# Performance work log

Hardware: AMD Instinct MI355X
Metric: run time of the kernel (lower is better)

## Reference

```python
import jax, jax.numpy as jnp
import numpy as np

N = 100000
E = 1600000
IN_DIM = 64
HID = 64


def _glorot(key, shape):
    fan_in, fan_out = shape[0], shape[1]
    lim = np.sqrt(6.0 / (fan_in + fan_out))
    return jax.random.uniform(key, shape, jnp.float32, -lim, lim)


def setup_inputs() -> dict:
    key = jax.random.key(0)
    ks = jax.random.split(key, 14)
    x = jax.random.normal(ks[0], (N, IN_DIM), jnp.float32)
    edge_index = jax.random.randint(ks[1], (2, E), 0, N, jnp.int64)
    dims = [(IN_DIM, HID), (HID, HID), (HID, HID), (HID, 1)]
    inp = {"x": x, "edge_index": edge_index}
    for i, (di, do) in enumerate(dims, start=1):
        inp[f"Wself{i}"] = _glorot(ks[2 + 3 * (i - 1)], (di, do))
        inp[f"Wneigh{i}"] = _glorot(ks[3 + 3 * (i - 1)], (di, do))
        inp[f"b{i}"] = jnp.zeros((do,), jnp.float32)
    return inp


def _gn_block(h, src, dst, deg_inv, Wself, Wneigh, b, act):
    # gather -> scatter-add -> mean -> dense transform (GraphConv-style)
    msg = h[src]                                           # [E, d]
    agg = jax.ops.segment_sum(msg, dst, num_segments=N)    # [N, d]
    agg = agg * deg_inv                                    # mean aggregation
    out = h @ Wself + agg @ Wneigh + b
    return act(out)


def reference(x, edge_index, Wself1, Wneigh1, b1, Wself2, Wneigh2, b2,
              Wself3, Wneigh3, b3, Wself4, Wneigh4, b4):
    src, dst = edge_index[0], edge_index[1]
    deg = jax.ops.segment_sum(jnp.ones((E,), x.dtype), dst, num_segments=N)
    deg_inv = (1.0 / jnp.maximum(deg, 1.0))[:, None]       # [N, 1]
    relu = jax.nn.relu
    h = _gn_block(x, src, dst, deg_inv, Wself1, Wneigh1, b1, relu)
    h = _gn_block(h, src, dst, deg_inv, Wself2, Wneigh2, b2, relu)
    h = _gn_block(h, src, dst, deg_inv, Wself3, Wneigh3, b3, relu)
    h = _gn_block(h, src, dst, deg_inv, Wself4, Wneigh4, b4, lambda z: z)
    return jax.nn.sigmoid(h)                               # [N, 1]
```

## Files before the change

### kernel.cpp

```cpp
#include <hip/hip_runtime.h>
#include <hip/hip_bf16.h>
#include <math.h>


using bfrag = __attribute__((ext_vector_type(8))) short;
using ffrag = __attribute__((ext_vector_type(4))) float;

#define BKT_SHIFT 9
#define BKT_NODES (1 << BKT_SHIFT)

__device__ __forceinline__ int load_idx32(const int* __restrict__ ei32, int is64,
                                          long long pos) {
    return is64 ? ei32[2 * pos] : ei32[pos];
}

__device__ __forceinline__ unsigned short f2b_rne(float f) {
    union { float f; unsigned u; } c;
    c.f = f;
    unsigned r = c.u + 0x7FFFu + ((c.u >> 16) & 1u);
    return (unsigned short)(r >> 16);
}

__device__ __forceinline__ float b2f(unsigned short u) {
    union { unsigned u; float f; } c;
    c.u = ((unsigned)u) << 16;
    return c.f;
}

__global__ void bprep_init_kernel(
    const float* __restrict__ Ws1, const float* __restrict__ Wn1,
    const float* __restrict__ Ws2, const float* __restrict__ Wn2,
    const float* __restrict__ Ws3, const float* __restrict__ Wn3,
    unsigned short* __restrict__ bthi, unsigned short* __restrict__ btlo,
    const int* __restrict__ ei, int* __restrict__ bktc, int* __restrict__ flag) {
    if (blockIdx.x == 0) {
        bktc[threadIdx.x] = 0;
        if (threadIdx.x == 0) {
            int allz = 1;
            for (int i = 0; i < 32; ++i)
                if (ei[2 * i + 1] != 0) allz = 0;
            *flag = allz;
        }
    }
    int i = blockIdx.x * 256 + threadIdx.x;
    if (i >= 3 * 8192) return;
    int layer = i >> 13;
    int j = i & 8191;
    int n = j >> 7, k = j & 127;
    const float* Ws = layer == 0 ? Ws1 : (layer == 1 ? Ws2 : Ws3);
    const float* Wn = layer == 0 ? Wn1 : (layer == 1 ? Wn2 : Wn3);
    float v = (k < 64) ? Ws[k * 64 + n] : Wn[(k - 64) * 64 + n];
    unsigned short hi = f2b_rne(v);
    bthi[i] = hi;
    btlo[i] = f2b_rne(v - b2f(hi));
}

__global__ void split_x_kernel(const float4* __restrict__ in, ushort4* __restrict__ hi,
                               int n4) {
    int i = blockIdx.x * blockDim.x + threadIdx.x;
    if (i >= n4) return;
    float4 v = in[i];
    ushort4 h;
    h.x = f2b_rne(v.x); h.y = f2b_rne(v.y); h.z = f2b_rne(v.z); h.w = f2b_rne(v.w);
    hi[i] = h;
}

__global__ __launch_bounds__(256) void binA_kernel(
    const int* __restrict__ ei32, const int* __restrict__ flagp,
    int* __restrict__ bktCnt, unsigned* __restrict__ bins, int E, int nbkt,
    int cap, int chunksz) {
    __shared__ int cnt[256];
    __shared__ int base[256];
    int is64 = *flagp;
    int elo = blockIdx.x * chunksz;
    int ehi = min(E, elo + chunksz);
    if (elo >= E) return;
    for (int i = threadIdx.x; i < nbkt; i += 256) cnt[i] = 0;
    __syncthreads();
    for (int e = elo + (int)threadIdx.x; e < ehi; e += 256) {
        int dst = load_idx32(ei32, is64, (long long)E + e);
        atomicAdd(&cnt[dst >> BKT_SHIFT], 1);
    }
    __syncthreads();
    for (int i = threadIdx.x; i < nbkt; i += 256) {
        base[i] = atomicAdd(&bktCnt[i], cnt[i]);
        cnt[i] = 0;
    }
    __syncthreads();
    for (int e = elo + (int)threadIdx.x; e < ehi; e += 256) {
        int dst = load_idx32(ei32, is64, (long long)E + e);
        int src = load_idx32(ei32, is64, e);
        int b = dst >> BKT_SHIFT;
        int r = atomicAdd(&cnt[b], 1);
        bins[(size_t)b * cap + base[b] + r] =
            ((unsigned)(dst & (BKT_NODES - 1)) << 23) | (unsigned)src;
    }
}

__global__ __launch_bounds__(256) void bucketCSR_kernel(
    const int* __restrict__ bktCnt, const unsigned* __restrict__ bins,
    int* __restrict__ off, int* __restrict__ offe, int* __restrict__ col,
    float* __restrict__ dinv, int N, int cap) {
    __shared__ int deg[BKT_NODES];
    __shared__ int loc[BKT_NODES];
    __shared__ int ssum[256];
    int b = blockIdx.x;
    int lo = b << BKT_SHIFT;
    int n = min(BKT_NODES, N - lo);
    for (int i = threadIdx.x; i < BKT_NODES; i += 256) deg[i] = 0;
    __syncthreads();
    int cnt = bktCnt[b];
    const unsigned* bb = bins + (size_t)b * cap;
    for (int i = threadIdx.x; i < cnt; i += 256)
        atomicAdd(&deg[bb[i] >> 23], 1);
    __syncthreads();
    int t = threadIdx.x;
    int d0 = deg[2 * t], d1 = deg[2 * t + 1];
    int s = d0 + d1;
    ssum[t] = s;
    __syncthreads();
    for (int o = 1; o < 256; o <<= 1) {
        int v = (t >= o) ? ssum[t - o] : 0;
        __syncthreads();
        ssum[t] += v;
        __syncthreads();
    }
    int excl = ssum[t] - s;
    loc[2 * t] = excl;
    loc[2 * t + 1] = excl + d0;
    __syncthreads();
    int base = b * cap;
    for (int i = threadIdx.x; i < n; i += 256) {
        int d = deg[i];
        off[lo + i] = base + loc[i];
        offe[lo + i] = base + loc[i] + d;
        dinv[lo + i] = 1.0f / fmaxf((float)d, 1.0f);
    }
    __syncthreads();
    for (int i = threadIdx.x; i < cnt; i += 256) {
        unsigned p = bb[i];
        int pos = atomicAdd(&loc[p >> 23], 1);
        col[base + pos] = (int)(p & 0x7FFFFFu);
    }
}

__global__ __launch_bounds__(256) void gather64_b16_kernel(
    const unsigned short* __restrict__ hb, const int* __restrict__ off,
    const int* __restrict__ offe, const int* __restrict__ col,
    const float* __restrict__ dinv, unsigned short* __restrict__ ghi, int N) {
    int wave = threadIdx.x >> 6;
    int lane = threadIdx.x & 63;
    int g = lane >> 4;
    int t = lane & 15;
    int n = blockIdx.x * 4 + wave;
    if (n >= N) return;
    int e = off[n], end = offe[n];
    float4 a0 = make_float4(0.f, 0.f, 0.f, 0.f);
    float4 a1 = make_float4(0.f, 0.f, 0.f, 0.f);
    float4 a2 = make_float4(0.f, 0.f, 0.f, 0.f);
    float4 a3 = make_float4(0.f, 0.f, 0.f, 0.f);
    for (; e + 16 <= end; e += 16) {
        int s0 = col[e + g];
        int s1 = col[e + 4 + g];
        int s2 = col[e + 8 + g];
        int s3 = col[e + 12 + g];
        ushort4 u0 = *(const ushort4*)&hb[(size_t)s0 * 64 + t * 4];
        ushort4 u1 = *(const ushort4*)&hb[(size_t)s1 * 64 + t * 4];
        ushort4 u2 = *(const ushort4*)&hb[(size_t)s2 * 64 + t * 4];
        ushort4 u3 = *(const ushort4*)&hb[(size_t)s3 * 64 + t * 4];
        a0.x += b2f(u0.x); a0.y += b2f(u0.y); a0.z += b2f(u0.z); a0.w += b2f(u0.w);
        a1.x += b2f(u1.x); a1.y += b2f(u1.y); a1.z += b2f(u1.z); a1.w += b2f(u1.w);
        a2.x += b2f(u2.x); a2.y += b2f(u2.y); a2.z += b2f(u2.z); a2.w += b2f(u2.w);
        a3.x += b2f(u3.x); a3.y += b2f(u3.y); a3.z += b2f(u3.z); a3.w += b2f(u3.w);
    }
    for (; e + 8 <= end; e += 8) {
        int s0 = col[e + g];
        int s1 = col[e + 4 + g];
        ushort4 u0 = *(const ushort4*)&hb[(size_t)s0 * 64 + t * 4];
        ushort4 u1 = *(const ushort4*)&hb[(size_t)s1 * 64 + t * 4];
        a0.x += b2f(u0.x); a0.y += b2f(u0.y); a0.z += b2f(u0.z); a0.w += b2f(u0.w);
        a1.x += b2f(u1.x); a1.y += b2f(u1.y); a1.z += b2f(u1.z); a1.w += b2f(u1.w);
    }
    for (; e < end; e += 4) {
        if (e + g < end) {
            int s0 = col[e + g];
            ushort4 u0 = *(const ushort4*)&hb[(size_t)s0 * 64 + t * 4];
            a2.x += b2f(u0.x); a2.y += b2f(u0.y); a2.z += b2f(u0.z); a2.w += b2f(u0.w);
        }
    }
    float4 acc;
    acc.x = (a0.x + a1.x) + (a2.x + a3.x);
    acc.y = (a0.y + a1.y) + (a2.y + a3.y);
    acc.z = (a0.z + a1.z) + (a2.z + a3.z);
    acc.w = (a0.w + a1.w) + (a2.w + a3.w);
#pragma unroll
    for (int m = 16; m <= 32; m <<= 1) {
        acc.x += __shfl_xor(acc.x, m, 64);
        acc.y += __shfl_xor(acc.y, m, 64);
        acc.z += __shfl_xor(acc.z, m, 64);
        acc.w += __shfl_xor(acc.w, m, 64);
    }
    if (g == 0) {
        float di = dinv[n];
        ushort4 h;
        h.x = f2b_rne(acc.x * di);
        h.y = f2b_rne(acc.y * di);
        h.z = f2b_rne(acc.z * di);
        h.w = f2b_rne(acc.w * di);
        *(ushort4*)&ghi[(size_t)n * 64 + t * 4] = h;
    }
}

__global__ __launch_bounds__(256) void dense_mfma_kernel(
    const unsigned short* __restrict__ Hhi, const unsigned short* __restrict__ Ghi,
    const unsigned short* __restrict__ Bthi, const unsigned short* __restrict__ Btlo,
    const float* __restrict__ b, unsigned short* __restrict__ Dhi, int N) {
    int lane = threadIdx.x & 63;
    int m = lane & 15, quad = lane >> 4;
    int wid = (blockIdx.x * blockDim.x + threadIdx.x) >> 6;
    int nw = (gridDim.x * blockDim.x) >> 6;
    bfrag bhi[4][4];
#pragma unroll
    for (int t = 0; t < 4; ++t)
#pragma unroll
        for (int c = 0; c < 4; ++c)
            bhi[t][c] = *(const bfrag*)(Bthi + (size_t)(t * 16 + m) * 128 + c * 32 + quad * 8);
    float bl[4];
#pragma unroll
    for (int t = 0; t < 4; ++t) bl[t] = b[t * 16 + m];
    int ngroups = (N + 15) >> 4;
    for (int g = wid; g < ngroups; g += nw) {
        int n0 = g << 4;
        int nr = n0 + m;
        if (nr > N - 1) nr = N - 1;
        const unsigned short* hrow = Hhi + (size_t)nr * 64 + quad * 8;
        const unsigned short* grow = Ghi + (size_t)nr * 64 + quad * 8;
        bfrag ah[4];
        ah[0] = *(const bfrag*)(hrow);
        ah[1] = *(const bfrag*)(hrow + 32);
        ah[2] = *(const bfrag*)(grow);
        ah[3] = *(const bfrag*)(grow + 32);
#pragma unroll
        for (int t = 0; t < 4; ++t) {
            ffrag acc = {bl[t], bl[t], bl[t], bl[t]};
#pragma unroll
            for (int c = 0; c < 4; ++c) {
                bfrag blo = *(const bfrag*)(Btlo + (size_t)(t * 16 + m) * 128 + c * 32 + quad * 8);
                acc = __builtin_amdgcn_mfma_f32_16x16x32_bf16(ah[c], bhi[t][c], acc, 0, 0, 0);
                acc = __builtin_amdgcn_mfma_f32_16x16x32_bf16(ah[c], blo, acc, 0, 0, 0);
            }
#pragma unroll
            for (int r = 0; r < 4; ++r) {
                int node = n0 + quad * 4 + r;
                if (node < N)
                    Dhi[(size_t)node * 64 + t * 16 + m] = f2b_rne(fmaxf(acc[r], 0.f));
            }
        }
    }
}

__global__ __launch_bounds__(256) void dense_mfma_last_kernel(
    const unsigned short* __restrict__ Hhi, const unsigned short* __restrict__ Ghi,
    const unsigned short* __restrict__ Bthi, const unsigned short* __restrict__ Btlo,
    const float* __restrict__ b, const float* __restrict__ Ws4,
    const float* __restrict__ Wn4, float* __restrict__ sbuf,
    float* __restrict__ gbuf, int N) {
    int lane = threadIdx.x & 63;
    int m = lane & 15, quad = lane >> 4;
    int wid = (blockIdx.x * blockDim.x + threadIdx.x) >> 6;
    int nw = (gridDim.x * blockDim.x) >> 6;
    bfrag bhi[4][4];
#pragma unroll
    for (int t = 0; t < 4; ++t)
#pragma unroll
        for (int c = 0; c < 4; ++c)
            bhi[t][c] = *(const bfrag*)(Bthi + (size_t)(t * 16 + m) * 128 + c * 32 + quad * 8);
    float bl[4], w4s[4], w4n[4];
#pragma unroll
    for (int t = 0; t < 4; ++t) {
        bl[t] = b[t * 16 + m];
        w4s[t] = Ws4[t * 16 + m];
        w4n[t] = Wn4[t * 16 + m];
    }
    int ngroups = (N + 15) >> 4;
    for (int g = wid; g < ngroups; g += nw) {
        int n0 = g << 4;
        int nr = n0 + m;
        if (nr > N - 1) nr = N - 1;
        const unsigned short* hrow = Hhi + (size_t)nr * 64 + quad * 8;
        const unsigned short* grow = Ghi + (size_t)nr * 64 + quad * 8;
        bfrag ah[4];
        ah[0] = *(const bfrag*)(hrow);
        ah[1] = *(const bfrag*)(hrow + 32);
        ah[2] = *(const bfrag*)(grow);
        ah[3] = *(const bfrag*)(grow + 32);
        ffrag accs[4];
#pragma unroll
        for (int t = 0; t < 4; ++t) {
            ffrag acc = {bl[t], bl[t], bl[t], bl[t]};
#pragma unroll
            for (int c = 0; c < 4; ++c) {
                bfrag blo = *(const bfrag*)(Btlo + (size_t)(t * 16 + m) * 128 + c * 32 + quad * 8);
                acc = __builtin_amdgcn_mfma_f32_16x16x32_bf16(ah[c], bhi[t][c], acc, 0, 0, 0);
                acc = __builtin_amdgcn_mfma_f32_16x16x32_bf16(ah[c], blo, acc, 0, 0, 0);
            }
            accs[t] = acc;
        }
#pragma unroll
        for (int r = 0; r < 4; ++r) {
            float ps = 0.f, pg = 0.f;
#pragma unroll
            for (int t = 0; t < 4; ++t) {
                float v = fmaxf(accs[t][r], 0.f);
                ps = fmaf(v, w4s[t], ps);
                pg = fmaf(v, w4n[t], pg);
            }
#pragma unroll
            for (int mask = 1; mask <= 8; mask <<= 1) {
                ps += __shfl_xor(ps, mask, 64);
                pg += __shfl_xor(pg, mask, 64);
            }
            int node = n0 + quad * 4 + r;
            if (m == 0 && node < N) {
                sbuf[node] = ps;
                gbuf[node] = pg;
            }
        }
    }
}

__global__ void final_kernel(const float* __restrict__ s, const float* __restrict__ dinv,
                             const float* __restrict__ g, const int* __restrict__ off,
                             const int* __restrict__ offe, const int* __restrict__ col,
                             const float* __restrict__ b4, float* __restrict__ out, int N) {
    int n = blockIdx.x * blockDim.x + threadIdx.x;
    if (n >= N) return;
    float a = 0.f;
    int e = off[n], end = offe[n];
    for (; e < end; ++e) a += g[col[e]];
    float z = s[n] + dinv[n] * a + b4[0];
    out[n] = 1.0f / (1.0f + expf(-z));
}

static inline int cdiv(long long a, long long b) { return (int)((a + b - 1) / b); }

extern "C" void kernel_launch(void* const* d_in, const int* in_sizes, int n_in,
                              void* d_out, int out_size, void* d_ws, size_t ws_size,
                              hipStream_t stream) {
    const float* x   = (const float*)d_in[0];
    const int*   ei  = (const int*)d_in[1];
    const float* Ws1 = (const float*)d_in[2];
    const float* Wn1 = (const float*)d_in[3];
    const float* b1  = (const float*)d_in[4];
    const float* Ws2 = (const float*)d_in[5];
    const float* Wn2 = (const float*)d_in[6];
    const float* b2  = (const float*)d_in[7];
    const float* Ws3 = (const float*)d_in[8];
    const float* Wn3 = (const float*)d_in[9];
    const float* b3  = (const float*)d_in[10];
    const float* Ws4 = (const float*)d_in[11];
    const float* Wn4 = (const float*)d_in[12];
    const float* b4  = (const float*)d_in[13];
    float* out = (float*)d_out;

    const int N = in_sizes[0] / 64;
    const int E = in_sizes[1] / 2;

    const int nbkt = cdiv(N, BKT_NODES);
    const int cap  = E / nbkt + E / nbkt / 8 + 64;

    unsigned* bins = (unsigned*)d_ws;
    int* col = (int*)(bins + (size_t)nbkt * cap);
    unsigned short* HhiA = (unsigned short*)(col + (size_t)nbkt * cap);
    unsigned short* HhiB = HhiA + (size_t)N * 64;
    unsigned short* Ghi  = HhiB + (size_t)N * 64;
    unsigned short* Bth  = Ghi + (size_t)N * 64;
    unsigned short* Btl  = Bth + 3 * 8192;
    float* dinv = (float*)(Btl + 3 * 8192);
    float* sbuf = dinv + N;
    float* gbuf = sbuf + N;
    int*   off  = (int*)(gbuf + N);
    int*   offe = off + N;
    int*   bktc = offe + N;
    int*   flag = bktc + 256;

    const int BT = 256;
    const int gridN  = cdiv(N, BT);
    const int gridNd = cdiv(N, 4);
    const int gridMM = cdiv(cdiv(N, 16), 4);
    const int binBlocks = 512;
    const int chunksz = cdiv(E, binBlocks);

    bprep_init_kernel<<<96, BT, 0, stream>>>(Ws1, Wn1, Ws2, Wn2, Ws3, Wn3,
                                             Bth, Btl, ei, bktc, flag);
    split_x_kernel<<<cdiv((long long)N * 16, BT), BT, 0, stream>>>(
        (const float4*)x, (ushort4*)HhiA, N * 16);

    binA_kernel<<<binBlocks, BT, 0, stream>>>(ei, flag, bktc, bins, E, nbkt, cap, chunksz);
    bucketCSR_kernel<<<nbkt, BT, 0, stream>>>(bktc, bins, off, offe, col, dinv, N, cap);

    gather64_b16_kernel<<<gridNd, BT, 0, stream>>>(HhiA, off, offe, col, dinv, Ghi, N);
    dense_mfma_kernel<<<gridMM, BT, 0, stream>>>(HhiA, Ghi, Bth, Btl, b1, HhiB, N);

    gather64_b16_kernel<<<gridNd, BT, 0, stream>>>(HhiB, off, offe, col, dinv, Ghi, N);
    dense_mfma_kernel<<<gridMM, BT, 0, stream>>>(HhiB, Ghi, Bth + 8192, Btl + 8192,
                                                 b2, HhiA, N);

    gather64_b16_kernel<<<gridNd, BT, 0, stream>>>(HhiA, off, offe, col, dinv, Ghi, N);
    dense_mfma_last_kernel<<<gridMM, BT, 0, stream>>>(HhiA, Ghi, Bth + 16384,
                                                      Btl + 16384, b3, Ws4, Wn4,
                                                      sbuf, gbuf, N);

    final_kernel<<<gridN, BT, 0, stream>>>(sbuf, dinv, gbuf, off, offe, col, b4, out, N);
}
```

Measured before the change: 415.9 us.

## Use smaller CSR buckets, fewer binning blocks, and fuse prep kernels

```diff
diff --git a/kernel.cpp b/kernel.cpp
--- a/kernel.cpp
+++ b/kernel.cpp
@@ -6,7 +6,7 @@
 using bfrag = __attribute__((ext_vector_type(8))) short;
 using ffrag = __attribute__((ext_vector_type(4))) float;
 
-#define BKT_SHIFT 9
+#define BKT_SHIFT 7
 #define BKT_NODES (1 << BKT_SHIFT)
 
 __device__ __forceinline__ int load_idx32(const int* __restrict__ ei32, int is64,
@@ -27,50 +27,52 @@
     return c.f;
 }
 
-__global__ void bprep_init_kernel(
+__global__ void prep_kernel(
     const float* __restrict__ Ws1, const float* __restrict__ Wn1,
     const float* __restrict__ Ws2, const float* __restrict__ Wn2,
     const float* __restrict__ Ws3, const float* __restrict__ Wn3,
     unsigned short* __restrict__ bthi, unsigned short* __restrict__ btlo,
-    const int* __restrict__ ei, int* __restrict__ bktc, int* __restrict__ flag) {
-    if (blockIdx.x == 0) {
-        bktc[threadIdx.x] = 0;
-        if (threadIdx.x == 0) {
+    const int* __restrict__ ei, int* __restrict__ bktc, int* __restrict__ flag,
+    const float4* __restrict__ x4, ushort4* __restrict__ hi4, int n4) {
+    int bid = blockIdx.x;
+    if (bid < 96) {
+        if (bid < 4) bktc[bid * 256 + threadIdx.x] = 0;
+        if (bid == 0 && threadIdx.x == 0) {
             int allz = 1;
             for (int i = 0; i < 32; ++i)
                 if (ei[2 * i + 1] != 0) allz = 0;
             *flag = allz;
         }
-    }
-    int i = blockIdx.x * 256 + threadIdx.x;
-    if (i >= 3 * 8192) return;
-    int layer = i >> 13;
-    int j = i & 8191;
-    int n = j >> 7, k = j & 127;
-    const float* Ws = layer == 0 ? Ws1 : (layer == 1 ? Ws2 : Ws3);
-    const float* Wn = layer == 0 ? Wn1 : (layer == 1 ? Wn2 : Wn3);
-    float v = (k < 64) ? Ws[k * 64 + n] : Wn[(k - 64) * 64 + n];
-    unsigned short hi = f2b_rne(v);
-    bthi[i] = hi;
-    btlo[i] = f2b_rne(v - b2f(hi));
-}
-
-__global__ void split_x_kernel(const float4* __restrict__ in, ushort4* __restrict__ hi,
-                               int n4) {
-    int i = blockIdx.x * blockDim.x + threadIdx.x;
-    if (i >= n4) return;
-    float4 v = in[i];
-    ushort4 h;
-    h.x = f2b_rne(v.x); h.y = f2b_rne(v.y); h.z = f2b_rne(v.z); h.w = f2b_rne(v.w);
-    hi[i] = h;
+        int i = bid * 256 + threadIdx.x;
+        if (i < 3 * 8192) {
+            int layer = i >> 13;
+            int j = i & 8191;
+            int n = j >> 7, k = j & 127;
+            const float* Ws = layer == 0 ? Ws1 : (layer == 1 ? Ws2 : Ws3);
+            const float* Wn = layer == 0 ? Wn1 : (layer == 1 ? Wn2 : Wn3);
+            float v = (k < 64) ? Ws[k * 64 + n] : Wn[(k - 64) * 64 + n];
+            unsigned short hi = f2b_rne(v);
+            bthi[i] = hi;
+            btlo[i] = f2b_rne(v - b2f(hi));
+        }
+    } else {
+        int i = (bid - 96) * 256 + threadIdx.x;
+        if (i < n4) {
+            float4 v = x4[i];
+            ushort4 h;
+            h.x = f2b_rne(v.x); h.y = f2b_rne(v.y);
+            h.z = f2b_rne(v.z); h.w = f2b_rne(v.w);
+            hi4[i] = h;
+        }
+    }
 }
 
 __global__ __launch_bounds__(256) void binA_kernel(
     const int* __restrict__ ei32, const int* __restrict__ flagp,
     int* __restrict__ bktCnt, unsigned* __restrict__ bins, int E, int nbkt,
     int cap, int chunksz) {
-    __shared__ int cnt[256];
-    __shared__ int base[256];
+    __shared__ int cnt[1024];
+    __shared__ int base[1024];
     int is64 = *flagp;
     int elo = blockIdx.x * chunksz;
     int ehi = min(E, elo + chunksz);
@@ -93,7 +95,7 @@
         int b = dst >> BKT_SHIFT;
         int r = atomicAdd(&cnt[b], 1);
         bins[(size_t)b * cap + base[b] + r] =
-            ((unsigned)(dst & (BKT_NODES - 1)) << 23) | (unsigned)src;
+            ((unsigned)(dst & (BKT_NODES - 1)) << 24) | (unsigned)src;
     }
 }
 
@@ -103,44 +105,40 @@
     float* __restrict__ dinv, int N, int cap) {
     __shared__ int deg[BKT_NODES];
     __shared__ int loc[BKT_NODES];
-    __shared__ int ssum[256];
+    __shared__ int ssum[BKT_NODES];
     int b = blockIdx.x;
     int lo = b << BKT_SHIFT;
     int n = min(BKT_NODES, N - lo);
-    for (int i = threadIdx.x; i < BKT_NODES; i += 256) deg[i] = 0;
+    int t = threadIdx.x;
+    if (t < BKT_NODES) deg[t] = 0;
     __syncthreads();
     int cnt = bktCnt[b];
     const unsigned* bb = bins + (size_t)b * cap;
-    for (int i = threadIdx.x; i < cnt; i += 256)
-        atomicAdd(&deg[bb[i] >> 23], 1);
-    __syncthreads();
-    int t = threadIdx.x;
-    int d0 = deg[2 * t], d1 = deg[2 * t + 1];
-    int s = d0 + d1;
-    ssum[t] = s;
-    __syncthreads();
-    for (int o = 1; o < 256; o <<= 1) {
-        int v = (t >= o) ? ssum[t - o] : 0;
+    for (int i = t; i < cnt; i += 256)
+        atomicAdd(&deg[bb[i] >> 24], 1);
+    __syncthreads();
+    if (t < BKT_NODES) ssum[t] = deg[t];
+    __syncthreads();
+    for (int o = 1; o < BKT_NODES; o <<= 1) {
+        int v = (t >= o && t < BKT_NODES) ? ssum[t - o] : 0;
         __syncthreads();
-        ssum[t] += v;
+        if (t < BKT_NODES) ssum[t] += v;
         __syncthreads();
     }
-    int excl = ssum[t] - s;
-    loc[2 * t] = excl;
-    loc[2 * t + 1] = excl + d0;
+    if (t < BKT_NODES) loc[t] = ssum[t] - deg[t];
     __syncthreads();
     int base = b * cap;
-    for (int i = threadIdx.x; i < n; i += 256) {
-        int d = deg[i];
-        off[lo + i] = base + loc[i];
-        offe[lo + i] = base + loc[i] + d;
-        dinv[lo + i] = 1.0f / fmaxf((float)d, 1.0f);
-    }
-    __syncthreads();
-    for (int i = threadIdx.x; i < cnt; i += 256) {
+    if (t < n) {
+        int d = deg[t];
+        off[lo + t] = base + loc[t];
+        offe[lo + t] = base + loc[t] + d;
+        dinv[lo + t] = 1.0f / fmaxf((float)d, 1.0f);
+    }
+    __syncthreads();
+    for (int i = t; i < cnt; i += 256) {
         unsigned p = bb[i];
-        int pos = atomicAdd(&loc[p >> 23], 1);
-        col[base + pos] = (int)(p & 0x7FFFFFu);
+        int pos = atomicAdd(&loc[p >> 24], 1);
+        col[base + pos] = (int)(p & 0xFFFFFFu);
     }
 }
 
@@ -382,19 +380,19 @@
     int*   off  = (int*)(gbuf + N);
     int*   offe = off + N;
     int*   bktc = offe + N;
-    int*   flag = bktc + 256;
+    int*   flag = bktc + 1024;
 
     const int BT = 256;
     const int gridN  = cdiv(N, BT);
     const int gridNd = cdiv(N, 4);
     const int gridMM = cdiv(cdiv(N, 16), 4);
-    const int binBlocks = 512;
+    const int binBlocks = 256;
     const int chunksz = cdiv(E, binBlocks);
-
-    bprep_init_kernel<<<96, BT, 0, stream>>>(Ws1, Wn1, Ws2, Wn2, Ws3, Wn3,
-                                             Bth, Btl, ei, bktc, flag);
-    split_x_kernel<<<cdiv((long long)N * 16, BT), BT, 0, stream>>>(
-        (const float4*)x, (ushort4*)HhiA, N * 16);
+    const int gridPrep = 96 + cdiv((long long)N * 16, BT);
+
+    prep_kernel<<<gridPrep, BT, 0, stream>>>(Ws1, Wn1, Ws2, Wn2, Ws3, Wn3,
+                                             Bth, Btl, ei, bktc, flag,
+                                             (const float4*)x, (ushort4*)HhiA, N * 16);
 
     binA_kernel<<<binBlocks, BT, 0, stream>>>(ei, flag, bktc, bins, E, nbkt, cap, chunksz);
     bucketCSR_kernel<<<nbkt, BT, 0, stream>>>(bktc, bins, off, offe, col, dinv, N, cap);
```

Measured after the change: 404.9 us. 2.6% less time.
